# Optimization experiments

Measured on AMD Instinct MI355X. Metric: run time of the kernel, lower is better.

Reference implementation:

```python
import jax, jax.numpy as jnp
import numpy as np

D_MODEL = 2048
NUM_HEADS = 32
NUM_KV_HEADS = 8
HEAD_DIM = D_MODEL // NUM_HEADS  # 64
GROUP = NUM_HEADS // NUM_KV_HEADS  # 4


def setup_inputs() -> dict:
    key = jax.random.key(0)
    ks = jax.random.split(key, 9)
    s = 1.0 / np.sqrt(D_MODEL)
    kv_dim = NUM_KV_HEADS * HEAD_DIM
    return {
        "x": jax.random.normal(ks[0], (2, 2048, D_MODEL), dtype=jnp.float32),
        "Wq": jax.random.normal(ks[1], (D_MODEL, D_MODEL), dtype=jnp.float32) * s,
        "bq": jnp.zeros((D_MODEL,), dtype=jnp.float32),
        "Wk": jax.random.normal(ks[2], (D_MODEL, kv_dim), dtype=jnp.float32) * s,
        "bk": jnp.zeros((kv_dim,), dtype=jnp.float32),
        "Wv": jax.random.normal(ks[3], (D_MODEL, kv_dim), dtype=jnp.float32) * s,
        "bv": jnp.zeros((kv_dim,), dtype=jnp.float32),
        "Wo": jax.random.normal(ks[4], (D_MODEL, D_MODEL), dtype=jnp.float32) * s,
        "bo": jnp.zeros((D_MODEL,), dtype=jnp.float32),
    }


def reference(x, Wq, bq, Wk, bk, Wv, bv, Wo, bo):
    B, S, _ = x.shape
    # projections
    q = (x @ Wq + bq).reshape(B, S, NUM_HEADS, HEAD_DIM).transpose(0, 2, 1, 3)      # [B,H,S,Dh]
    k = (x @ Wk + bk).reshape(B, S, NUM_KV_HEADS, HEAD_DIM).transpose(0, 2, 1, 3)   # [B,Hkv,S,Dh]
    v = (x @ Wv + bv).reshape(B, S, NUM_KV_HEADS, HEAD_DIM).transpose(0, 2, 1, 3)
    # expand KV heads to match query heads (repeat_interleave along head dim)
    k = jnp.repeat(k, GROUP, axis=1)  # [B,H,S,Dh]
    v = jnp.repeat(v, GROUP, axis=1)
    scale = 1.0 / np.sqrt(HEAD_DIM).astype(np.float32)
    scores = jnp.einsum('bhqd,bhkd->bhqk', q, k) * scale  # [B,H,S,S]
    attn = jax.nn.softmax(scores, axis=-1)
    out = jnp.einsum('bhqk,bhkd->bhqd', attn, v)          # [B,H,S,Dh]
    out = out.transpose(0, 2, 1, 3).reshape(B, S, NUM_HEADS * HEAD_DIM)
    return out @ Wo + bo
```

## Files before the change

### kernel.cpp

```cpp
#include <hip/hip_runtime.h>
#include <stdint.h>

typedef unsigned short u16;
typedef unsigned int u32;
typedef short bf16x8 __attribute__((ext_vector_type(8)));
typedef float f32x4 __attribute__((ext_vector_type(4)));
typedef u32 u32x2 __attribute__((ext_vector_type(2)));

#define GLOAD_LDS16(gptr, lptr)                                                \
  __builtin_amdgcn_global_load_lds(                                            \
      (__attribute__((address_space(1))) void*)(gptr),                         \
      (__attribute__((address_space(3))) void*)(lptr), 16, 0, 0)

#if __has_builtin(__builtin_amdgcn_exp2f)
#define EXP2F(x) __builtin_amdgcn_exp2f(x)
#else
#define EXP2F(x) exp2f(x)
#endif

__device__ __forceinline__ u16 f2bf(float f) {
  union { float f; uint32_t u; } v; v.f = f;
  return (u16)((v.u + 0x7fffu + ((v.u >> 16) & 1u)) >> 16);
}
__device__ __forceinline__ float bf2f(u16 h) {
  union { uint32_t u; float f; } v; v.u = ((uint32_t)h) << 16;
  return v.f;
}
__device__ __forceinline__ u32 cvt_pk_bf16(float lo, float hi) {
  u32 r;
  asm("v_cvt_pk_bf16_f32 %0, %1, %2" : "=v"(r) : "v"(lo), "v"(hi));
  return r;
}

__global__ void k_conv_bf16(const float* __restrict__ src, u16* __restrict__ dst, int n8) {
  int i = blockIdx.x * blockDim.x + threadIdx.x;
  if (i >= n8) return;
  const float4* s = (const float4*)src + (size_t)i * 2;
  float4 a = s[0], b = s[1];
  uint4 o;
  o.x = (uint32_t)f2bf(a.x) | ((uint32_t)f2bf(a.y) << 16);
  o.y = (uint32_t)f2bf(a.z) | ((uint32_t)f2bf(a.w) << 16);
  o.z = (uint32_t)f2bf(b.x) | ((uint32_t)f2bf(b.y) << 16);
  o.w = (uint32_t)f2bf(b.z) | ((uint32_t)f2bf(b.w) << 16);
  ((uint4*)dst)[i] = o;
}

__global__ void k_transpose_bf16(const float* __restrict__ src, u16* __restrict__ dst,
                                 int R, int C) {
  __shared__ float tile[32][33];
  int cb = blockIdx.x * 32, rb = blockIdx.y * 32;
  int tx = threadIdx.x, ty = threadIdx.y;
#pragma unroll
  for (int j = 0; j < 4; ++j)
    tile[ty + j * 8][tx] = src[(size_t)(rb + ty + j * 8) * C + cb + tx];
  __syncthreads();
#pragma unroll
  for (int j = 0; j < 4; ++j)
    dst[(size_t)(cb + ty + j * 8) * R + rb + tx] = f2bf(tile[tx][ty + j * 8]);
}

__global__ void k_transpose_v(const u16* __restrict__ cqkv, u16* __restrict__ vt) {
  __shared__ u16 tile[32][34];
  int st = blockIdx.x, dt = blockIdx.y, bk = blockIdx.z;
  int b = bk >> 3, kvh = bk & 7;
  int tx = threadIdx.x, ty = threadIdx.y;
  const u16* src = cqkv + (size_t)(b * 2048 + st * 32) * 3072 + 2560 + kvh * 64 + dt * 32;
#pragma unroll
  for (int j = 0; j < 4; ++j)
    tile[ty + j * 8][tx] = src[(size_t)(ty + j * 8) * 3072 + tx];
  __syncthreads();
  u16* dst = vt + ((size_t)(bk * 64 + dt * 32)) * 2048 + st * 32;
#pragma unroll
  for (int j = 0; j < 4; ++j)
    dst[(size_t)(ty + j * 8) * 2048 + tx] = tile[tx][ty + j * 8];
}

template <bool BF16OUT>
__global__ __launch_bounds__(256) void k_gemm_bt(
    const u16* __restrict__ A, const u16* __restrict__ Bt,
    const float* __restrict__ bias, void* __restrict__ Cptr,
    int M, int N, int K, int gx, int nwg) {
  __shared__ u16 As[2][128 * 32];
  __shared__ u16 Bs[2][128 * 32];
  const int t = threadIdx.x;
  const int lane = t & 63;
  const int w = t >> 6, wr = w >> 1, wc = w & 1;
  const int bid = blockIdx.x;
  const int cpx = nwg >> 3;
  const int swz = (bid & 7) * cpx + (bid >> 3);
  const int brow = (swz / gx) * 128, bcol = (swz % gx) * 128;
  const int g = lane >> 4, q = lane & 15;

  f32x4 acc[4][4] = {};
  const int srow = t >> 2;
  const int sj = t & 3;
  const int nkt = K >> 5;

  auto stage = [&](int bb, int kt_) {
#pragma unroll
    for (int i = 0; i < 2; ++i) {
      int row = srow + i * 64;
      int jsrc = sj ^ ((row >> 1) & 3);
      const u16* ga = A + (size_t)(brow + row) * K + kt_ * 32 + jsrc * 8;
      const u16* gb = Bt + (size_t)(bcol + row) * K + kt_ * 32 + jsrc * 8;
      GLOAD_LDS16(ga, (char*)(&As[bb][0]) + i * 4096 + t * 16);
      GLOAD_LDS16(gb, (char*)(&Bs[bb][0]) + i * 4096 + t * 16);
    }
  };

  stage(0, 0);
  __syncthreads();
  int cur = 0;

  for (int kt = 0; kt < nkt; ++kt) {
    if (kt < nkt - 1) stage(cur ^ 1, kt + 1);
    const u16* Ac = As[cur];
    const u16* Bc = Bs[cur];
    bf16x8 a[4], b[4];
#pragma unroll
    for (int mt = 0; mt < 4; ++mt) {
      int row = wr * 64 + mt * 16 + q;
      int pos = g ^ ((row >> 1) & 3);
      a[mt] = *(const bf16x8*)(Ac + row * 32 + pos * 8);
    }
#pragma unroll
    for (int nt = 0; nt < 4; ++nt) {
      int row = wc * 64 + nt * 16 + q;
      int pos = g ^ ((row >> 1) & 3);
      b[nt] = *(const bf16x8*)(Bc + row * 32 + pos * 8);
    }
    __builtin_amdgcn_s_setprio(1);
#pragma unroll
    for (int mt = 0; mt < 4; ++mt)
#pragma unroll
      for (int nt = 0; nt < 4; ++nt)
        acc[mt][nt] = __builtin_amdgcn_mfma_f32_16x16x32_bf16(a[mt], b[nt], acc[mt][nt], 0, 0, 0);
    __builtin_amdgcn_s_setprio(0);
    __syncthreads();
    cur ^= 1;
  }
#pragma unroll
  for (int nt = 0; nt < 4; ++nt) {
    int col = bcol + wc * 64 + nt * 16 + q;
    float bv_ = bias[col];
#pragma unroll
    for (int mt = 0; mt < 4; ++mt) {
#pragma unroll
      for (int r = 0; r < 4; ++r) {
        int row = brow + wr * 64 + mt * 16 + g * 4 + r;
        float val = acc[mt][nt][r] + bv_;
        if (BF16OUT)
          ((u16*)Cptr)[(size_t)row * N + col] = f2bf(val);
        else
          ((float*)Cptr)[(size_t)row * N + col] = val;
      }
    }
  }
}

#define LOG2E 1.44269504088896340736f
__global__ __launch_bounds__(256) void k_attn(const u16* __restrict__ qkv,
                                              const u16* __restrict__ vt,
                                              u16* __restrict__ out) {
  const int qt = blockIdx.x, h = blockIdx.y, b = blockIdx.z;
  const int kvh = h >> 2;
  const int t = threadIdx.x, lane = t & 63, w = t >> 6;
  const int g = lane >> 4, q16 = lane & 15;
  const int LDQ = 3072;

  __shared__ u16 Ksh[2][64 * 64];
  __shared__ u16 Vsh[2][64 * 64];
  __shared__ u16 Psh[4][16 * 72] __attribute__((aligned(16)));

  bf16x8 qf[2][2];
#pragma unroll
  for (int sub = 0; sub < 2; ++sub) {
    const size_t qrow = (size_t)(b * 2048 + qt * 128 + sub * 64 + w * 16 + q16);
#pragma unroll
    for (int c = 0; c < 2; ++c) {
      bf16x8 tmp = *(const bf16x8*)(qkv + qrow * LDQ + h * 64 + c * 32 + g * 8);
#pragma unroll
      for (int i = 0; i < 8; ++i)
        tmp[i] = (short)f2bf(bf2f((u16)tmp[i]) * 0.125f);
      qf[sub][c] = tmp;
    }
  }

  f32x4 acc[2][4] = {};
  float m_run[2], l_run[2];
  m_run[0] = m_run[1] = -__builtin_inff();
  l_run[0] = l_run[1] = 0.f;

  const int kbase = b * 2048;
  const int koff = 2048 + kvh * 64;
  const u16* vtb = vt + (size_t)((b * 8 + kvh) * 64) * 2048;
  const int srow = t >> 3;
  const int sj = t & 7;

  auto stage = [&](int bb, int kt_) {
#pragma unroll
    for (int p = 0; p < 2; ++p) {
      int row = srow + p * 32;
      int cx = sj ^ (row & 7);
      const u16* gk = qkv + (size_t)(kbase + kt_ * 64 + row) * LDQ + koff + cx * 8;
      GLOAD_LDS16(gk, (char*)(&Ksh[bb][0]) + p * 4096 + t * 16);
      const u16* gv = vtb + (size_t)row * 2048 + kt_ * 64 + cx * 8;
      GLOAD_LDS16(gv, (char*)(&Vsh[bb][0]) + p * 4096 + t * 16);
    }
  };

  stage(0, 0);
  __syncthreads();
  int cur = 0;

  for (int kt = 0; kt < 32; ++kt) {
    if (kt < 31) stage(cur ^ 1, kt + 1);
    const u16* Kc = Ksh[cur];
    const u16* Vc = Vsh[cur];

    f32x4 sc[2][4] = {};
    __builtin_amdgcn_s_setprio(1);
#pragma unroll
    for (int c = 0; c < 2; ++c) {
#pragma unroll
      for (int nt = 0; nt < 4; ++nt) {
        int row = nt * 16 + q16;
        bf16x8 kf = *(const bf16x8*)(Kc + row * 64 + (((c * 4 + g) ^ (row & 7)) << 3));
        sc[0][nt] = __builtin_amdgcn_mfma_f32_16x16x32_bf16(kf, qf[0][c], sc[0][nt], 0, 0, 0);
        sc[1][nt] = __builtin_amdgcn_mfma_f32_16x16x32_bf16(kf, qf[1][c], sc[1][nt], 0, 0, 0);
      }
    }
    __builtin_amdgcn_s_setprio(0);

    bf16x8 pf[2][2];
#pragma unroll
    for (int sub = 0; sub < 2; ++sub) {
      float mt_ = sc[sub][0][0];
#pragma unroll
      for (int nt = 0; nt < 4; ++nt)
#pragma unroll
        for (int r = 0; r < 4; ++r)
          mt_ = fmaxf(mt_, sc[sub][nt][r]);
      mt_ = fmaxf(mt_, __shfl_xor(mt_, 16, 64));
      mt_ = fmaxf(mt_, __shfl_xor(mt_, 32, 64));
      if (__any(mt_ > m_run[sub])) {
        float mn = fmaxf(m_run[sub], mt_);
        float alpha = EXP2F((m_run[sub] - mn) * LOG2E);
        m_run[sub] = mn;
        l_run[sub] *= alpha;
#pragma unroll
        for (int r = 0; r < 4; ++r) {
          float ar = __shfl(alpha, g * 4 + r, 64);
#pragma unroll
          for (int dt = 0; dt < 4; ++dt) acc[sub][dt][r] *= ar;
        }
      }
      float mL = m_run[sub] * LOG2E;
      float lt = 0.f;
#pragma unroll
      for (int nt = 0; nt < 4; ++nt)
#pragma unroll
        for (int r = 0; r < 4; ++r) {
          float p_ = EXP2F(fmaf(sc[sub][nt][r], LOG2E, -mL));
          sc[sub][nt][r] = p_;
          lt += p_;
        }
      lt += __shfl_xor(lt, 16, 64);
      lt += __shfl_xor(lt, 32, 64);
      l_run[sub] += lt;
      u16* prow = &Psh[w][q16 * 72];
#pragma unroll
      for (int nt = 0; nt < 4; ++nt) {
        u32x2 pk;
        pk.x = cvt_pk_bf16(sc[sub][nt][0], sc[sub][nt][1]);
        pk.y = cvt_pk_bf16(sc[sub][nt][2], sc[sub][nt][3]);
        *(u32x2*)(prow + nt * 16 + g * 4) = pk;
      }
      pf[sub][0] = *(const bf16x8*)(&Psh[w][q16 * 72 + g * 8]);
      pf[sub][1] = *(const bf16x8*)(&Psh[w][q16 * 72 + 32 + g * 8]);
    }

    __builtin_amdgcn_s_setprio(1);
#pragma unroll
    for (int c = 0; c < 2; ++c) {
      int kc = c * 4 + g;
#pragma unroll
      for (int dt = 0; dt < 4; ++dt) {
        int d = dt * 16 + q16;
        bf16x8 vf = *(const bf16x8*)(Vc + d * 64 + ((kc ^ (d & 7)) << 3));
        acc[0][dt] = __builtin_amdgcn_mfma_f32_16x16x32_bf16(pf[0][c], vf, acc[0][dt], 0, 0, 0);
        acc[1][dt] = __builtin_amdgcn_mfma_f32_16x16x32_bf16(pf[1][c], vf, acc[1][dt], 0, 0, 0);
      }
    }
    __builtin_amdgcn_s_setprio(0);

    __syncthreads();
    cur ^= 1;
  }

#pragma unroll
  for (int sub = 0; sub < 2; ++sub)
#pragma unroll
    for (int r = 0; r < 4; ++r) {
      float linv = 1.0f / __shfl(l_run[sub], g * 4 + r, 64);
      size_t orow = (size_t)(b * 2048 + qt * 128 + sub * 64 + w * 16 + g * 4 + r);
#pragma unroll
      for (int dt = 0; dt < 4; ++dt)
        out[orow * 2048 + h * 64 + dt * 16 + q16] = f2bf(acc[sub][dt][r] * linv);
    }
}

extern "C" void kernel_launch(void* const* d_in, const int* in_sizes, int n_in,
                              void* d_out, int out_size, void* d_ws, size_t ws_size,
                              hipStream_t stream) {
  const float* x  = (const float*)d_in[0];
  const float* Wq = (const float*)d_in[1];
  const float* bq = (const float*)d_in[2];
  const float* Wk = (const float*)d_in[3];
  const float* bk = (const float*)d_in[4];
  const float* Wv = (const float*)d_in[5];
  const float* bv = (const float*)d_in[6];
  const float* Wo = (const float*)d_in[7];
  const float* bo = (const float*)d_in[8];
  float* out = (float*)d_out;

  char* ws = (char*)d_ws;
  u16*   xb    = (u16*)(ws + 0);
  u16*   wqkvT = (u16*)(ws + 16777216);
  u16*   woT   = (u16*)(ws + 29360128);
  float* bqkv  = (float*)(ws + 37748736);
  u16*   cqkv  = (u16*)(ws + 37761024);
  u16*   aout  = (u16*)(ws + 62926848);
  u16*   vtb   = xb;
  (void)ws_size; (void)in_sizes; (void)n_in; (void)out_size;

  hipMemcpyAsync(bqkv, bq, 2048 * sizeof(float), hipMemcpyDeviceToDevice, stream);
  hipMemcpyAsync(bqkv + 2048, bk, 512 * sizeof(float), hipMemcpyDeviceToDevice, stream);
  hipMemcpyAsync(bqkv + 2560, bv, 512 * sizeof(float), hipMemcpyDeviceToDevice, stream);

  k_conv_bf16<<<4096, 256, 0, stream>>>(x, xb, 1048576);
  dim3 tb(32, 8);
  k_transpose_bf16<<<dim3(64, 64), tb, 0, stream>>>(Wq, wqkvT, 2048, 2048);
  k_transpose_bf16<<<dim3(16, 64), tb, 0, stream>>>(Wk, wqkvT + 2048 * 2048, 2048, 512);
  k_transpose_bf16<<<dim3(16, 64), tb, 0, stream>>>(Wv, wqkvT + 2560 * 2048, 2048, 512);
  k_transpose_bf16<<<dim3(64, 64), tb, 0, stream>>>(Wo, woT, 2048, 2048);

  k_gemm_bt<true><<<768, 256, 0, stream>>>(xb, wqkvT, bqkv, cqkv, 4096, 3072, 2048, 24, 768);
  k_transpose_v<<<dim3(64, 2, 16), tb, 0, stream>>>(cqkv, vtb);
  k_attn<<<dim3(16, 32, 2), 256, 0, stream>>>(cqkv, vtb, aout);
  k_gemm_bt<false><<<512, 256, 0, stream>>>(aout, woT, bo, out, 4096, 2048, 2048, 16, 512);
}
```

Measured before the change: 380.3 us.

## Double query rows per attention block to reuse staged K/V tiles

Each attention block now handles 256 query rows instead of 128, in two passes of two 64-row sub-tiles over each staged K/V tile. This halves the grid and the total K/V global-to-LDS traffic per head. Staging pointers are also precomputed and incremented, replacing per-iteration address arithmetic. The cost is more registers for Q fragments and accumulators, which may lower occupancy, and only 512 blocks to spread across the CUs.

```diff
diff --git a/kernel.cpp b/kernel.cpp
--- a/kernel.cpp
+++ b/kernel.cpp
@@ -172,141 +172,146 @@
   __shared__ u16 Vsh[2][64 * 64];
   __shared__ u16 Psh[4][16 * 72] __attribute__((aligned(16)));
 
-  bf16x8 qf[2][2];
-#pragma unroll
-  for (int sub = 0; sub < 2; ++sub) {
-    const size_t qrow = (size_t)(b * 2048 + qt * 128 + sub * 64 + w * 16 + q16);
+  bf16x8 qf[4][2];
+#pragma unroll
+  for (int s = 0; s < 4; ++s) {
+    const size_t qrow = (size_t)(b * 2048 + qt * 256 + s * 64 + w * 16 + q16);
 #pragma unroll
     for (int c = 0; c < 2; ++c) {
       bf16x8 tmp = *(const bf16x8*)(qkv + qrow * LDQ + h * 64 + c * 32 + g * 8);
 #pragma unroll
       for (int i = 0; i < 8; ++i)
         tmp[i] = (short)f2bf(bf2f((u16)tmp[i]) * 0.125f);
-      qf[sub][c] = tmp;
+      qf[s][c] = tmp;
     }
   }
 
-  f32x4 acc[2][4] = {};
-  float m_run[2], l_run[2];
-  m_run[0] = m_run[1] = -__builtin_inff();
-  l_run[0] = l_run[1] = 0.f;
+  f32x4 acc[4][4] = {};
+  float m_run[4], l_run[4];
+#pragma unroll
+  for (int s = 0; s < 4; ++s) { m_run[s] = -__builtin_inff(); l_run[s] = 0.f; }
 
   const int kbase = b * 2048;
   const int koff = 2048 + kvh * 64;
   const u16* vtb = vt + (size_t)((b * 8 + kvh) * 64) * 2048;
   const int srow = t >> 3;
   const int sj = t & 7;
-
-  auto stage = [&](int bb, int kt_) {
-#pragma unroll
-    for (int p = 0; p < 2; ++p) {
-      int row = srow + p * 32;
-      int cx = sj ^ (row & 7);
-      const u16* gk = qkv + (size_t)(kbase + kt_ * 64 + row) * LDQ + koff + cx * 8;
-      GLOAD_LDS16(gk, (char*)(&Ksh[bb][0]) + p * 4096 + t * 16);
-      const u16* gv = vtb + (size_t)row * 2048 + kt_ * 64 + cx * 8;
-      GLOAD_LDS16(gv, (char*)(&Vsh[bb][0]) + p * 4096 + t * 16);
-    }
+  const int cx = sj ^ (srow & 7);
+
+  const u16* gk = qkv + (size_t)(kbase + srow) * LDQ + koff + cx * 8;
+  const u16* gv = vtb + (size_t)srow * 2048 + cx * 8;
+
+  auto stage = [&](int bb) {
+    GLOAD_LDS16(gk,               (char*)(&Ksh[bb][0]) + t * 16);
+    GLOAD_LDS16(gk + 32 * LDQ,    (char*)(&Ksh[bb][0]) + 4096 + t * 16);
+    GLOAD_LDS16(gv,               (char*)(&Vsh[bb][0]) + t * 16);
+    GLOAD_LDS16(gv + 32 * 2048,   (char*)(&Vsh[bb][0]) + 4096 + t * 16);
   };
 
-  stage(0, 0);
+  stage(0);
+  gk += 64 * LDQ; gv += 64;
   __syncthreads();
   int cur = 0;
 
   for (int kt = 0; kt < 32; ++kt) {
-    if (kt < 31) stage(cur ^ 1, kt + 1);
+    if (kt < 31) { stage(cur ^ 1); gk += 64 * LDQ; gv += 64; }
     const u16* Kc = Ksh[cur];
     const u16* Vc = Vsh[cur];
 
-    f32x4 sc[2][4] = {};
-    __builtin_amdgcn_s_setprio(1);
-#pragma unroll
-    for (int c = 0; c < 2; ++c) {
-#pragma unroll
-      for (int nt = 0; nt < 4; ++nt) {
-        int row = nt * 16 + q16;
-        bf16x8 kf = *(const bf16x8*)(Kc + row * 64 + (((c * 4 + g) ^ (row & 7)) << 3));
-        sc[0][nt] = __builtin_amdgcn_mfma_f32_16x16x32_bf16(kf, qf[0][c], sc[0][nt], 0, 0, 0);
-        sc[1][nt] = __builtin_amdgcn_mfma_f32_16x16x32_bf16(kf, qf[1][c], sc[1][nt], 0, 0, 0);
-      }
-    }
-    __builtin_amdgcn_s_setprio(0);
-
-    bf16x8 pf[2][2];
-#pragma unroll
-    for (int sub = 0; sub < 2; ++sub) {
-      float mt_ = sc[sub][0][0];
-#pragma unroll
-      for (int nt = 0; nt < 4; ++nt)
-#pragma unroll
-        for (int r = 0; r < 4; ++r)
-          mt_ = fmaxf(mt_, sc[sub][nt][r]);
-      mt_ = fmaxf(mt_, __shfl_xor(mt_, 16, 64));
-      mt_ = fmaxf(mt_, __shfl_xor(mt_, 32, 64));
-      if (__any(mt_ > m_run[sub])) {
-        float mn = fmaxf(m_run[sub], mt_);
-        float alpha = EXP2F((m_run[sub] - mn) * LOG2E);
-        m_run[sub] = mn;
-        l_run[sub] *= alpha;
-#pragma unroll
-        for (int r = 0; r < 4; ++r) {
-          float ar = __shfl(alpha, g * 4 + r, 64);
-#pragma unroll
-          for (int dt = 0; dt < 4; ++dt) acc[sub][dt][r] *= ar;
+#pragma unroll
+    for (int p2 = 0; p2 < 2; ++p2) {
+      const int s0 = p2 * 2, s1 = p2 * 2 + 1;
+      f32x4 sc[2][4] = {};
+      __builtin_amdgcn_s_setprio(1);
+#pragma unroll
+      for (int c = 0; c < 2; ++c) {
+#pragma unroll
+        for (int nt = 0; nt < 4; ++nt) {
+          int row = nt * 16 + q16;
+          bf16x8 kf = *(const bf16x8*)(Kc + row * 64 + (((c * 4 + g) ^ (row & 7)) << 3));
+          sc[0][nt] = __builtin_amdgcn_mfma_f32_16x16x32_bf16(kf, qf[s0][c], sc[0][nt], 0, 0, 0);
+          sc[1][nt] = __builtin_amdgcn_mfma_f32_16x16x32_bf16(kf, qf[s1][c], sc[1][nt], 0, 0, 0);
         }
       }
-      float mL = m_run[sub] * LOG2E;
-      float lt = 0.f;
-#pragma unroll
-      for (int nt = 0; nt < 4; ++nt)
-#pragma unroll
-        for (int r = 0; r < 4; ++r) {
-          float p_ = EXP2F(fmaf(sc[sub][nt][r], LOG2E, -mL));
-          sc[sub][nt][r] = p_;
-          lt += p_;
+      __builtin_amdgcn_s_setprio(0);
+
+      bf16x8 pf[2][2];
+#pragma unroll
+      for (int i2 = 0; i2 < 2; ++i2) {
+        const int s = p2 * 2 + i2;
+        float mt_ = sc[i2][0][0];
+#pragma unroll
+        for (int nt = 0; nt < 4; ++nt)
+#pragma unroll
+          for (int r = 0; r < 4; ++r)
+            mt_ = fmaxf(mt_, sc[i2][nt][r]);
+        mt_ = fmaxf(mt_, __shfl_xor(mt_, 16, 64));
+        mt_ = fmaxf(mt_, __shfl_xor(mt_, 32, 64));
+        if (__any(mt_ > m_run[s])) {
+          float mn = fmaxf(m_run[s], mt_);
+          float alpha = EXP2F((m_run[s] - mn) * LOG2E);
+          m_run[s] = mn;
+          l_run[s] *= alpha;
+#pragma unroll
+          for (int r = 0; r < 4; ++r) {
+            float ar = __shfl(alpha, g * 4 + r, 64);
+#pragma unroll
+            for (int dt = 0; dt < 4; ++dt) acc[s][dt][r] *= ar;
+          }
         }
-      lt += __shfl_xor(lt, 16, 64);
-      lt += __shfl_xor(lt, 32, 64);
-      l_run[sub] += lt;
-      u16* prow = &Psh[w][q16 * 72];
-#pragma unroll
-      for (int nt = 0; nt < 4; ++nt) {
-        u32x2 pk;
-        pk.x = cvt_pk_bf16(sc[sub][nt][0], sc[sub][nt][1]);
-        pk.y = cvt_pk_bf16(sc[sub][nt][2], sc[sub][nt][3]);
-        *(u32x2*)(prow + nt * 16 + g * 4) = pk;
+        float mL = m_run[s] * LOG2E;
+        float lt = 0.f;
+#pragma unroll
+        for (int nt = 0; nt < 4; ++nt)
+#pragma unroll
+          for (int r = 0; r < 4; ++r) {
+            float p_ = EXP2F(fmaf(sc[i2][nt][r], LOG2E, -mL));
+            sc[i2][nt][r] = p_;
+            lt += p_;
+          }
+        lt += __shfl_xor(lt, 16, 64);
+        lt += __shfl_xor(lt, 32, 64);
+        l_run[s] += lt;
+        u16* prow = &Psh[w][q16 * 72];
+#pragma unroll
+        for (int nt = 0; nt < 4; ++nt) {
+          u32x2 pk;
+          pk.x = cvt_pk_bf16(sc[i2][nt][0], sc[i2][nt][1]);
+          pk.y = cvt_pk_bf16(sc[i2][nt][2], sc[i2][nt][3]);
+          *(u32x2*)(prow + nt * 16 + g * 4) = pk;
+        }
+        pf[i2][0] = *(const bf16x8*)(&Psh[w][q16 * 72 + g * 8]);
+        pf[i2][1] = *(const bf16x8*)(&Psh[w][q16 * 72 + 32 + g * 8]);
       }
-      pf[sub][0] = *(const bf16x8*)(&Psh[w][q16 * 72 + g * 8]);
-      pf[sub][1] = *(const bf16x8*)(&Psh[w][q16 * 72 + 32 + g * 8]);
-    }
-
-    __builtin_amdgcn_s_setprio(1);
-#pragma unroll
-    for (int c = 0; c < 2; ++c) {
-      int kc = c * 4 + g;
-#pragma unroll
-      for (int dt = 0; dt < 4; ++dt) {
-        int d = dt * 16 + q16;
-        bf16x8 vf = *(const bf16x8*)(Vc + d * 64 + ((kc ^ (d & 7)) << 3));
-        acc[0][dt] = __builtin_amdgcn_mfma_f32_16x16x32_bf16(pf[0][c], vf, acc[0][dt], 0, 0, 0);
-        acc[1][dt] = __builtin_amdgcn_mfma_f32_16x16x32_bf16(pf[1][c], vf, acc[1][dt], 0, 0, 0);
+
+      __builtin_amdgcn_s_setprio(1);
+#pragma unroll
+      for (int c = 0; c < 2; ++c) {
+        int kc = c * 4 + g;
+#pragma unroll
+        for (int dt = 0; dt < 4; ++dt) {
+          int d = dt * 16 + q16;
+          bf16x8 vf = *(const bf16x8*)(Vc + d * 64 + ((kc ^ (d & 7)) << 3));
+          acc[s0][dt] = __builtin_amdgcn_mfma_f32_16x16x32_bf16(pf[0][c], vf, acc[s0][dt], 0, 0, 0);
+          acc[s1][dt] = __builtin_amdgcn_mfma_f32_16x16x32_bf16(pf[1][c], vf, acc[s1][dt], 0, 0, 0);
+        }
       }
-    }
-    __builtin_amdgcn_s_setprio(0);
+      __builtin_amdgcn_s_setprio(0);
+    }
 
     __syncthreads();
     cur ^= 1;
   }
 
 #pragma unroll
-  for (int sub = 0; sub < 2; ++sub)
+  for (int s = 0; s < 4; ++s)
 #pragma unroll
     for (int r = 0; r < 4; ++r) {
-      float linv = 1.0f / __shfl(l_run[sub], g * 4 + r, 64);
-      size_t orow = (size_t)(b * 2048 + qt * 128 + sub * 64 + w * 16 + g * 4 + r);
+      float linv = 1.0f / __shfl(l_run[s], g * 4 + r, 64);
+      size_t orow = (size_t)(b * 2048 + qt * 256 + s * 64 + w * 16 + g * 4 + r);
 #pragma unroll
       for (int dt = 0; dt < 4; ++dt)
-        out[orow * 2048 + h * 64 + dt * 16 + q16] = f2bf(acc[sub][dt][r] * linv);
+        out[orow * 2048 + h * 64 + dt * 16 + q16] = f2bf(acc[s][dt][r] * linv);
     }
 }
 
@@ -347,6 +352,6 @@
 
   k_gemm_bt<true><<<768, 256, 0, stream>>>(xb, wqkvT, bqkv, cqkv, 4096, 3072, 2048, 24, 768);
   k_transpose_v<<<dim3(64, 2, 16), tb, 0, stream>>>(cqkv, vtb);
-  k_attn<<<dim3(16, 32, 2), 256, 0, stream>>>(cqkv, vtb, aout);
+  k_attn<<<dim3(8, 32, 2), 256, 0, stream>>>(cqkv, vtb, aout);
   k_gemm_bt<false><<<512, 256, 0, stream>>>(aout, woT, bo, out, 4096, 2048, 2048, 16, 512);
 }
```

Measured after the change: 372.5 us. -2.1%, faster.
